# Optimization experiments

Measured on AMD Instinct MI355X. Metric: run time of the kernel, lower is better.

The kernel has to match this reference:

```python
import jax, jax.numpy as jnp
import numpy as np

N_NODES = 50000
N_EDGES = 800000
HIDDEN = 100
NUM_TASKS = 128
NUM_GRAPHS = 2000
ATOM_DIMS = [119, 5, 12, 12, 10, 6, 6, 2, 2]  # OGB full_atom_feature_dims
EPS = 1e-16  # stands in for PyG's clamp(min=0) so that pow(-1) stays finite


def setup_inputs() -> dict:
    key = jax.random.key(0)
    ks = jax.random.split(key, 8)
    x = jax.random.randint(ks[0], (N_NODES, 9), 0, 2, dtype=jnp.int32)
    edge_index = jax.random.randint(ks[1], (2, N_EDGES), 0, N_NODES, dtype=jnp.int32)
    batch = jnp.sort(jax.random.randint(ks[2], (N_NODES,), 0, NUM_GRAPHS, dtype=jnp.int32))
    s = 1.0 / np.sqrt(HIDDEN)
    atom_emb = jax.random.normal(ks[3], (sum(ATOM_DIMS), HIDDEN), jnp.float32)
    W1 = jax.random.normal(ks[4], (HIDDEN, HIDDEN), jnp.float32) * s
    b1 = jnp.zeros((HIDDEN,), jnp.float32)
    W2 = jax.random.normal(ks[5], (HIDDEN, HIDDEN), jnp.float32) * s
    b2 = jnp.zeros((HIDDEN,), jnp.float32)
    Wlin = jax.random.normal(ks[6], (HIDDEN, NUM_TASKS), jnp.float32) * s
    blin = jnp.zeros((NUM_TASKS,), jnp.float32)
    return dict(x=x, edge_index=edge_index, batch=batch, atom_emb=atom_emb,
                W1=W1, b1=b1, W2=W2, b2=b2, Wlin=Wlin, blin=blin)


def reference(x, edge_index, batch, atom_emb, W1, b1, W2, b2, Wlin, blin):
    # --- AtomEncoder: sum of per-feature categorical embeddings ---
    offsets = jnp.asarray(np.concatenate([[0], np.cumsum(ATOM_DIMS)[:-1]]), jnp.int32)
    h = jnp.take(atom_emb, x + offsets[None, :], axis=0).sum(axis=1)  # [N, H]

    # --- GCN normalization with self-loops (gcn_norm, edge_weight=None) ---
    loops = jnp.arange(N_NODES, dtype=edge_index.dtype)
    row = jnp.concatenate([edge_index[0], loops])  # source
    col = jnp.concatenate([edge_index[1], loops])  # target
    ew = jnp.ones(row.shape[0], jnp.float32)
    deg = jax.ops.segment_sum(ew, col, num_segments=N_NODES)  # in-degree incl self-loop
    dinv = jnp.where(deg > 0, deg ** -0.5, 0.0)
    norm = dinv[row] * ew * dinv[col]  # [E+N]
    cnt = jnp.maximum(deg, 1.0)  # messages per target node (for mean)

    def gcn_conv(h, W, b):
        msg = norm[:, None] * (h @ W)[row]  # [E+N, H]
        # PowerMeanAggregation(p=-1): clamp(0,100).pow(-1) -> mean -> clamp(0,100).pow(-1)
        msg = jnp.clip(msg, EPS, 100.0) ** (-1.0)
        agg = jax.ops.segment_sum(msg, col, num_segments=N_NODES) / cnt[:, None]
        return jnp.clip(agg, EPS, 100.0) ** (-1.0) + b

    h = jax.nn.relu(gcn_conv(h, W1, b1))
    h = gcn_conv(h, W2, b2)

    # --- global_mean_pool over batch ---
    gcnt = jax.ops.segment_sum(jnp.ones((N_NODES,), jnp.float32), batch, num_segments=NUM_GRAPHS)
    pooled = jax.ops.segment_sum(h, batch, num_segments=NUM_GRAPHS) / jnp.maximum(gcnt, 1.0)[:, None]

    return pooled @ Wlin + blin  # [NUM_GRAPHS, NUM_TASKS]
```

## Files before the change

### kernel.cpp

```cpp
#include <hip/hip_runtime.h>

#define N_NODES   50000
#define N_EDGES   800000
#define HIDDEN    100
#define NUM_TASKS 128
#define NUM_GRAPHS 2000
#define EPS 1e-16f

static __device__ __forceinline__ float rcp_fast(float v) {
    return __builtin_amdgcn_rcpf(v);
}
static __device__ __forceinline__ float invclip(float v) {
    return rcp_fast(fminf(fmaxf(v, EPS), 100.0f));
}
static __device__ __forceinline__ unsigned pack_bf16x2(float a, float b) {
    unsigned r;
    asm("v_cvt_pk_bf16_f32 %0, %1, %2" : "=v"(r) : "v"(a), "v"(b));
    return r;
}

__global__ void init_kernel(int* __restrict__ deg, int* __restrict__ cursor) {
    int i = blockIdx.x * blockDim.x + threadIdx.x;
    if (i < N_NODES) { deg[i] = 1; cursor[i] = 0; }
}

__global__ void deg_count_kernel(const int* __restrict__ col, int* __restrict__ deg) {
    int e = blockIdx.x * blockDim.x + threadIdx.x;
    if (e < N_EDGES) atomicAdd(&deg[col[e]], 1);
}

__global__ void blk_sum_kernel(const int* __restrict__ deg, int* __restrict__ bsum) {
    int i = blockIdx.x * 256 + threadIdx.x;
    int v = (i < N_NODES) ? (deg[i] - 1) : 0;
#pragma unroll
    for (int off = 32; off > 0; off >>= 1) v += __shfl_down(v, off, 64);
    __shared__ int ws[4];
    if ((threadIdx.x & 63) == 0) ws[threadIdx.x >> 6] = v;
    __syncthreads();
    if (threadIdx.x == 0) bsum[blockIdx.x] = ws[0] + ws[1] + ws[2] + ws[3];
}

__global__ void bsum_scan_kernel(int* __restrict__ bsum, int nblk) {
    __shared__ int buf[256];
    int t = threadIdx.x;
    int v = (t < nblk) ? bsum[t] : 0;
    buf[t] = v;
    __syncthreads();
    for (int off = 1; off < 256; off <<= 1) {
        int x = (t >= off) ? buf[t - off] : 0;
        __syncthreads();
        buf[t] += x;
        __syncthreads();
    }
    if (t < nblk) bsum[t] = buf[t] - v;
}

__global__ void blk_scan_kernel(const int* __restrict__ deg, const int* __restrict__ bbase,
                                int* __restrict__ csr_off, float* __restrict__ dinv) {
    __shared__ int buf[256];
    int t = threadIdx.x;
    int i = blockIdx.x * 256 + t;
    int dv = (i < N_NODES) ? deg[i] : 1;
    int v = (i < N_NODES) ? (dv - 1) : 0;
    buf[t] = v;
    __syncthreads();
    for (int off = 1; off < 256; off <<= 1) {
        int x = (t >= off) ? buf[t - off] : 0;
        __syncthreads();
        buf[t] += x;
        __syncthreads();
    }
    if (i < N_NODES) {
        csr_off[i] = bbase[blockIdx.x] + buf[t] - v;
        dinv[i] = 1.0f / sqrtf((float)dv);
    } else if (i == N_NODES) {
        csr_off[N_NODES] = N_EDGES;
    }
}

__global__ void scatter_kernel(const int* __restrict__ row, const int* __restrict__ col,
                               const int* __restrict__ csr_off, int* __restrict__ cursor,
                               const float* __restrict__ dinv, int2* __restrict__ csr_pack) {
    int e = blockIdx.x * blockDim.x + threadIdx.x;
    if (e >= N_EDGES) return;
    int s = row[e], d = col[e];
    int pos = csr_off[d] + atomicAdd(&cursor[d], 1);
    int2 p;
    p.x = s;
    p.y = __float_as_int(dinv[s] * dinv[d]);
    csr_pack[pos] = p;
}

__global__ void encoder_kernel(const int* __restrict__ x, const float* __restrict__ emb,
                               float* __restrict__ h) {
    int n = blockIdx.x;
    int d = threadIdx.x;
    if (d >= HIDDEN) return;
    const int offs[9] = {0, 119, 124, 136, 148, 158, 164, 170, 172};
    float acc = 0.0f;
#pragma unroll
    for (int f = 0; f < 9; ++f) {
        int idx = x[n * 9 + f] + offs[f];
        acc += emb[idx * HIDDEN + d];
    }
    h[n * HIDDEN + d] = acc;
}

#define MM_NODES 64
#define WL_PAD   10032
__global__ __launch_bounds__(512) void matmul_kernel(const float* __restrict__ h,
                                                     const float* __restrict__ W,
                                                     unsigned* __restrict__ outb) {
    __shared__ float Wl[WL_PAD];
    __shared__ float hl[MM_NODES * HIDDEN];
    int tid = threadIdx.x;
    int nb = blockIdx.x * MM_NODES;

    for (int i = tid; i < WL_PAD; i += 512)
        Wl[i] = (i < HIDDEN * HIDDEN) ? W[i] : 0.0f;
    for (int i = tid; i < MM_NODES * HIDDEN; i += 512) {
        int n = i / HIDDEN;
        hl[i] = (nb + n < N_NODES) ? h[(size_t)(nb + n) * HIDDEN + (i % HIDDEN)] : 0.0f;
    }
    __syncthreads();

    int tx = tid & 31;
    int ty = tid >> 5;

    float4 acc[4];
#pragma unroll
    for (int jn = 0; jn < 4; ++jn) acc[jn] = make_float4(0.f, 0.f, 0.f, 0.f);

    for (int kk = 0; kk < HIDDEN; kk += 4) {
        float hs[4][4];
#pragma unroll
        for (int jn = 0; jn < 4; ++jn) {
            float4 hv = *(const float4*)&hl[(ty + 16 * jn) * HIDDEN + kk];
            hs[jn][0] = hv.x; hs[jn][1] = hv.y; hs[jn][2] = hv.z; hs[jn][3] = hv.w;
        }
#pragma unroll
        for (int dk = 0; dk < 4; ++dk) {
            float4 wv = *(const float4*)&Wl[(kk + dk) * HIDDEN + 4 * tx];
#pragma unroll
            for (int jn = 0; jn < 4; ++jn) {
                acc[jn].x += hs[jn][dk] * wv.x;
                acc[jn].y += hs[jn][dk] * wv.y;
                acc[jn].z += hs[jn][dk] * wv.z;
                acc[jn].w += hs[jn][dk] * wv.w;
            }
        }
    }

    if (tx < 25) {
#pragma unroll
        for (int jn = 0; jn < 4; ++jn) {
            int n = nb + ty + 16 * jn;
            if (n < N_NODES) {
                uint2 pk;
                pk.x = pack_bf16x2(acc[jn].x, acc[jn].y);
                pk.y = pack_bf16x2(acc[jn].z, acc[jn].w);
                *(uint2*)&outb[(size_t)n * 50 + 2 * tx] = pk;
            }
        }
    }
}

__global__ __launch_bounds__(256) void agg_kernel(
        const unsigned* __restrict__ hw16, const int* __restrict__ csr_off,
        const int2* __restrict__ csr_pack, const float* __restrict__ dinv,
        const int* __restrict__ deg, const float* __restrict__ bias,
        float* __restrict__ out, int relu) {
    int wid  = (blockIdx.x * blockDim.x + threadIdx.x) >> 6;
    int lane = threadIdx.x & 63;
    if (wid >= N_NODES) return;
    int n = wid;
    bool act = lane < 50;

    float cnt = (float)deg[n];
    float thr = 100.0f * cnt;
    float dn  = dinv[n];
    float nrm = dn * dn;

    float2 acc;
    if (act) {
        unsigned u = hw16[(size_t)n * 50 + lane];
        acc.x = invclip(nrm * __int_as_float(u << 16));
        acc.y = invclip(nrm * __int_as_float(u & 0xFFFF0000u));
    } else {
        acc.x = 3.0e38f;
        acc.y = 3.0e38f;
    }

    int beg = csr_off[n], end = csr_off[n + 1];
    int i = beg;
    for (; i + 4 <= end; i += 4) {
        int2 p0 = csr_pack[i];
        int2 p1 = csr_pack[i + 1];
        int2 p2 = csr_pack[i + 2];
        int2 p3 = csr_pack[i + 3];
        unsigned u0 = act ? hw16[(size_t)p0.x * 50 + lane] : 0u;
        unsigned u1 = act ? hw16[(size_t)p1.x * 50 + lane] : 0u;
        unsigned u2 = act ? hw16[(size_t)p2.x * 50 + lane] : 0u;
        unsigned u3 = act ? hw16[(size_t)p3.x * 50 + lane] : 0u;
        float w0 = __int_as_float(p0.y), w1 = __int_as_float(p1.y);
        float w2 = __int_as_float(p2.y), w3 = __int_as_float(p3.y);
        acc.x += invclip(w0 * __int_as_float(u0 << 16));
        acc.y += invclip(w0 * __int_as_float(u0 & 0xFFFF0000u));
        acc.x += invclip(w1 * __int_as_float(u1 << 16));
        acc.y += invclip(w1 * __int_as_float(u1 & 0xFFFF0000u));
        acc.x += invclip(w2 * __int_as_float(u2 << 16));
        acc.y += invclip(w2 * __int_as_float(u2 & 0xFFFF0000u));
        acc.x += invclip(w3 * __int_as_float(u3 << 16));
        acc.y += invclip(w3 * __int_as_float(u3 & 0xFFFF0000u));
        if (__all((acc.x >= thr) & (acc.y >= thr))) { i = end; break; }
    }
    for (; i < end; ++i) {
        int2 p = csr_pack[i];
        unsigned u = act ? hw16[(size_t)p.x * 50 + lane] : 0u;
        float w = __int_as_float(p.y);
        acc.x += invclip(w * __int_as_float(u << 16));
        acc.y += invclip(w * __int_as_float(u & 0xFFFF0000u));
    }

    if (act) {
        float rcnt = rcp_fast(cnt);
        float2 o;
        o.x = invclip(acc.x * rcnt) + bias[2 * lane];
        o.y = invclip(acc.y * rcnt) + bias[2 * lane + 1];
        if (relu) { o.x = fmaxf(o.x, 0.f); o.y = fmaxf(o.y, 0.f); }
        *(float2*)&out[(size_t)n * HIDDEN + 2 * lane] = o;
    }
}

__global__ void pool_final_kernel(const float* __restrict__ h, const int* __restrict__ batch,
                                  const float* __restrict__ Wlin, const float* __restrict__ blin,
                                  float* __restrict__ out) {
    int g = blockIdx.x;
    int t = threadIdx.x;
    __shared__ float pl[HIDDEN];

    int lo = 0, hi = N_NODES;
    while (lo < hi) { int mid = (lo + hi) >> 1; if (batch[mid] < g) lo = mid + 1; else hi = mid; }
    int start = lo;
    hi = N_NODES;
    while (lo < hi) { int mid = (lo + hi) >> 1; if (batch[mid] < g + 1) lo = mid + 1; else hi = mid; }
    int end = lo;

    float inv = 1.0f / fmaxf((float)(end - start), 1.0f);
    if (t < HIDDEN) {
        float acc = 0.f;
        for (int n = start; n < end; ++n) acc += h[(size_t)n * HIDDEN + t];
        pl[t] = acc * inv;
    }
    __syncthreads();

    float o = 0.f;
#pragma unroll 4
    for (int j = 0; j < HIDDEN; ++j) o += pl[j] * Wlin[j * NUM_TASKS + t];
    out[(size_t)g * NUM_TASKS + t] = o + blin[t];
}

extern "C" void kernel_launch(void* const* d_in, const int* in_sizes, int n_in,
                              void* d_out, int out_size, void* d_ws, size_t ws_size,
                              hipStream_t stream) {
    const int*   x     = (const int*)d_in[0];
    const int*   ei    = (const int*)d_in[1];
    const int*   batch = (const int*)d_in[2];
    const float* emb   = (const float*)d_in[3];
    const float* W1    = (const float*)d_in[4];
    const float* b1    = (const float*)d_in[5];
    const float* W2    = (const float*)d_in[6];
    const float* b2    = (const float*)d_in[7];
    const float* Wlin  = (const float*)d_in[8];
    const float* blin  = (const float*)d_in[9];
    float* out = (float*)d_out;

    const int* row = ei;
    const int* col = ei + N_EDGES;

    char* ws = (char*)d_ws;
    auto alloc = [&](size_t bytes) -> char* {
        char* p = ws;
        ws += (bytes + 255) & ~(size_t)255;
        return p;
    };
    int*      deg      = (int*)     alloc((size_t)N_NODES * 4);
    int*      cursor   = (int*)     alloc((size_t)N_NODES * 4);
    int*      csr_off  = (int*)     alloc((size_t)(N_NODES + 1) * 4);
    float*    dinv     = (float*)   alloc((size_t)N_NODES * 4);
    int2*     csr_pack = (int2*)    alloc((size_t)N_EDGES * 8);
    float*    bufA     = (float*)   alloc((size_t)N_NODES * HIDDEN * 4);
    unsigned* hw16     = (unsigned*)alloc((size_t)N_NODES * 50 * 4);
    int*      bsum     = (int*)     alloc(256 * 4);

    const int SCAN_BLOCKS = (N_NODES + 255) / 256;

    init_kernel<<<(N_NODES + 255) / 256, 256, 0, stream>>>(deg, cursor);
    deg_count_kernel<<<(N_EDGES + 255) / 256, 256, 0, stream>>>(col, deg);
    blk_sum_kernel<<<SCAN_BLOCKS, 256, 0, stream>>>(deg, bsum);
    bsum_scan_kernel<<<1, 256, 0, stream>>>(bsum, SCAN_BLOCKS);
    blk_scan_kernel<<<SCAN_BLOCKS, 256, 0, stream>>>(deg, bsum, csr_off, dinv);
    scatter_kernel<<<(N_EDGES + 255) / 256, 256, 0, stream>>>(row, col, csr_off, cursor, dinv,
                                                              csr_pack);
    encoder_kernel<<<N_NODES, 128, 0, stream>>>(x, emb, bufA);

    const int MM_BLOCKS = (N_NODES + MM_NODES - 1) / MM_NODES;
    matmul_kernel<<<MM_BLOCKS, 512, 0, stream>>>(bufA, W1, hw16);
    agg_kernel<<<(N_NODES + 3) / 4, 256, 0, stream>>>(hw16, csr_off, csr_pack,
                                                      dinv, deg, b1, bufA, 1);
    matmul_kernel<<<MM_BLOCKS, 512, 0, stream>>>(bufA, W2, hw16);
    agg_kernel<<<(N_NODES + 3) / 4, 256, 0, stream>>>(hw16, csr_off, csr_pack,
                                                      dinv, deg, b2, bufA, 0);

    pool_final_kernel<<<NUM_GRAPHS, 128, 0, stream>>>(bufA, batch, Wlin, blin, out);
}
```

Before: 305.4 us.

## Fuse atom encoder into first matmul, drop early exit, use nontemporal CSR loads

The atom encoder is folded into the first GEMM kernel, so embeddings are built directly in shared memory and the encoder output never round-trips through global memory. The aggregation kernel drops its saturation-based early-exit vote and reads CSR pairs with nontemporal 64-bit loads. It also writes output with nontemporal stores and launches 128-thread blocks of two wavefronts. Removing the early exit means every edge is always processed, which may cost time on nodes whose sums saturate early.

```diff
diff --git a/kernel.cpp b/kernel.cpp
--- a/kernel.cpp
+++ b/kernel.cpp
@@ -91,39 +91,11 @@
     csr_pack[pos] = p;
 }
 
-__global__ void encoder_kernel(const int* __restrict__ x, const float* __restrict__ emb,
-                               float* __restrict__ h) {
-    int n = blockIdx.x;
-    int d = threadIdx.x;
-    if (d >= HIDDEN) return;
-    const int offs[9] = {0, 119, 124, 136, 148, 158, 164, 170, 172};
-    float acc = 0.0f;
-#pragma unroll
-    for (int f = 0; f < 9; ++f) {
-        int idx = x[n * 9 + f] + offs[f];
-        acc += emb[idx * HIDDEN + d];
-    }
-    h[n * HIDDEN + d] = acc;
-}
-
 #define MM_NODES 64
 #define WL_PAD   10032
-__global__ __launch_bounds__(512) void matmul_kernel(const float* __restrict__ h,
-                                                     const float* __restrict__ W,
-                                                     unsigned* __restrict__ outb) {
-    __shared__ float Wl[WL_PAD];
-    __shared__ float hl[MM_NODES * HIDDEN];
-    int tid = threadIdx.x;
-    int nb = blockIdx.x * MM_NODES;
-
-    for (int i = tid; i < WL_PAD; i += 512)
-        Wl[i] = (i < HIDDEN * HIDDEN) ? W[i] : 0.0f;
-    for (int i = tid; i < MM_NODES * HIDDEN; i += 512) {
-        int n = i / HIDDEN;
-        hl[i] = (nb + n < N_NODES) ? h[(size_t)(nb + n) * HIDDEN + (i % HIDDEN)] : 0.0f;
-    }
-    __syncthreads();
-
+
+static __device__ __forceinline__ void gemm_tile(const float* Wl, const float* hl,
+                                                 unsigned* __restrict__ outb, int nb, int tid) {
     int tx = tid & 31;
     int ty = tid >> 5;
 
@@ -165,7 +137,60 @@
     }
 }
 
-__global__ __launch_bounds__(256) void agg_kernel(
+__global__ __launch_bounds__(512) void mm_enc_kernel(const int* __restrict__ x,
+                                                     const float* __restrict__ emb,
+                                                     const float* __restrict__ W,
+                                                     unsigned* __restrict__ outb) {
+    __shared__ float Wl[WL_PAD];
+    __shared__ float hl[MM_NODES * HIDDEN];
+    __shared__ int   xl[MM_NODES * 9];
+    int tid = threadIdx.x;
+    int nb = blockIdx.x * MM_NODES;
+
+    for (int i = tid; i < WL_PAD; i += 512)
+        Wl[i] = (i < HIDDEN * HIDDEN) ? W[i] : 0.0f;
+    for (int i = tid; i < MM_NODES * 9; i += 512) {
+        int n = i / 9, gn = nb + n;
+        xl[i] = (gn < N_NODES) ? x[gn * 9 + (i - n * 9)] : -1;
+    }
+    __syncthreads();
+
+    const int offs[9] = {0, 119, 124, 136, 148, 158, 164, 170, 172};
+    for (int i = tid; i < MM_NODES * HIDDEN; i += 512) {
+        int n = i / HIDDEN, d = i - n * HIDDEN;
+        float acc = 0.0f;
+        if (xl[n * 9] >= 0) {
+#pragma unroll
+            for (int f = 0; f < 9; ++f)
+                acc += emb[(size_t)(xl[n * 9 + f] + offs[f]) * HIDDEN + d];
+        }
+        hl[i] = acc;
+    }
+    __syncthreads();
+
+    gemm_tile(Wl, hl, outb, nb, tid);
+}
+
+__global__ __launch_bounds__(512) void matmul_kernel(const float* __restrict__ h,
+                                                     const float* __restrict__ W,
+                                                     unsigned* __restrict__ outb) {
+    __shared__ float Wl[WL_PAD];
+    __shared__ float hl[MM_NODES * HIDDEN];
+    int tid = threadIdx.x;
+    int nb = blockIdx.x * MM_NODES;
+
+    for (int i = tid; i < WL_PAD; i += 512)
+        Wl[i] = (i < HIDDEN * HIDDEN) ? W[i] : 0.0f;
+    for (int i = tid; i < MM_NODES * HIDDEN; i += 512) {
+        int n = i / HIDDEN;
+        hl[i] = (nb + n < N_NODES) ? h[(size_t)(nb + n) * HIDDEN + (i % HIDDEN)] : 0.0f;
+    }
+    __syncthreads();
+
+    gemm_tile(Wl, hl, outb, nb, tid);
+}
+
+__global__ __launch_bounds__(128) void agg_kernel(
         const unsigned* __restrict__ hw16, const int* __restrict__ csr_off,
         const int2* __restrict__ csr_pack, const float* __restrict__ dinv,
         const int* __restrict__ deg, const float* __restrict__ bias,
@@ -177,33 +202,33 @@
     bool act = lane < 50;
 
     float cnt = (float)deg[n];
-    float thr = 100.0f * cnt;
     float dn  = dinv[n];
     float nrm = dn * dn;
 
-    float2 acc;
+    float2 acc = make_float2(0.f, 0.f);
     if (act) {
         unsigned u = hw16[(size_t)n * 50 + lane];
         acc.x = invclip(nrm * __int_as_float(u << 16));
         acc.y = invclip(nrm * __int_as_float(u & 0xFFFF0000u));
-    } else {
-        acc.x = 3.0e38f;
-        acc.y = 3.0e38f;
-    }
-
+    }
+
+    const long long* packs = (const long long*)csr_pack;
     int beg = csr_off[n], end = csr_off[n + 1];
     int i = beg;
     for (; i + 4 <= end; i += 4) {
-        int2 p0 = csr_pack[i];
-        int2 p1 = csr_pack[i + 1];
-        int2 p2 = csr_pack[i + 2];
-        int2 p3 = csr_pack[i + 3];
-        unsigned u0 = act ? hw16[(size_t)p0.x * 50 + lane] : 0u;
-        unsigned u1 = act ? hw16[(size_t)p1.x * 50 + lane] : 0u;
-        unsigned u2 = act ? hw16[(size_t)p2.x * 50 + lane] : 0u;
-        unsigned u3 = act ? hw16[(size_t)p3.x * 50 + lane] : 0u;
-        float w0 = __int_as_float(p0.y), w1 = __int_as_float(p1.y);
-        float w2 = __int_as_float(p2.y), w3 = __int_as_float(p3.y);
+        long long q0 = __builtin_nontemporal_load(&packs[i]);
+        long long q1 = __builtin_nontemporal_load(&packs[i + 1]);
+        long long q2 = __builtin_nontemporal_load(&packs[i + 2]);
+        long long q3 = __builtin_nontemporal_load(&packs[i + 3]);
+        int s0 = (int)q0, s1 = (int)q1, s2 = (int)q2, s3 = (int)q3;
+        unsigned u0 = act ? hw16[(size_t)s0 * 50 + lane] : 0u;
+        unsigned u1 = act ? hw16[(size_t)s1 * 50 + lane] : 0u;
+        unsigned u2 = act ? hw16[(size_t)s2 * 50 + lane] : 0u;
+        unsigned u3 = act ? hw16[(size_t)s3 * 50 + lane] : 0u;
+        float w0 = __int_as_float((int)(q0 >> 32));
+        float w1 = __int_as_float((int)(q1 >> 32));
+        float w2 = __int_as_float((int)(q2 >> 32));
+        float w3 = __int_as_float((int)(q3 >> 32));
         acc.x += invclip(w0 * __int_as_float(u0 << 16));
         acc.y += invclip(w0 * __int_as_float(u0 & 0xFFFF0000u));
         acc.x += invclip(w1 * __int_as_float(u1 << 16));
@@ -212,23 +237,24 @@
         acc.y += invclip(w2 * __int_as_float(u2 & 0xFFFF0000u));
         acc.x += invclip(w3 * __int_as_float(u3 << 16));
         acc.y += invclip(w3 * __int_as_float(u3 & 0xFFFF0000u));
-        if (__all((acc.x >= thr) & (acc.y >= thr))) { i = end; break; }
     }
     for (; i < end; ++i) {
-        int2 p = csr_pack[i];
-        unsigned u = act ? hw16[(size_t)p.x * 50 + lane] : 0u;
-        float w = __int_as_float(p.y);
+        long long q = __builtin_nontemporal_load(&packs[i]);
+        int s = (int)q;
+        unsigned u = act ? hw16[(size_t)s * 50 + lane] : 0u;
+        float w = __int_as_float((int)(q >> 32));
         acc.x += invclip(w * __int_as_float(u << 16));
         acc.y += invclip(w * __int_as_float(u & 0xFFFF0000u));
     }
 
     if (act) {
         float rcnt = rcp_fast(cnt);
-        float2 o;
-        o.x = invclip(acc.x * rcnt) + bias[2 * lane];
-        o.y = invclip(acc.y * rcnt) + bias[2 * lane + 1];
-        if (relu) { o.x = fmaxf(o.x, 0.f); o.y = fmaxf(o.y, 0.f); }
-        *(float2*)&out[(size_t)n * HIDDEN + 2 * lane] = o;
+        float ox = invclip(acc.x * rcnt) + bias[2 * lane];
+        float oy = invclip(acc.y * rcnt) + bias[2 * lane + 1];
+        if (relu) { ox = fmaxf(ox, 0.f); oy = fmaxf(oy, 0.f); }
+        unsigned long long w = (unsigned long long)__float_as_uint(ox)
+                             | ((unsigned long long)__float_as_uint(oy) << 32);
+        __builtin_nontemporal_store(w, (unsigned long long*)&out[(size_t)n * HIDDEN + 2 * lane]);
     }
 }
 
@@ -302,14 +328,13 @@
     blk_scan_kernel<<<SCAN_BLOCKS, 256, 0, stream>>>(deg, bsum, csr_off, dinv);
     scatter_kernel<<<(N_EDGES + 255) / 256, 256, 0, stream>>>(row, col, csr_off, cursor, dinv,
                                                               csr_pack);
-    encoder_kernel<<<N_NODES, 128, 0, stream>>>(x, emb, bufA);
 
     const int MM_BLOCKS = (N_NODES + MM_NODES - 1) / MM_NODES;
-    matmul_kernel<<<MM_BLOCKS, 512, 0, stream>>>(bufA, W1, hw16);
-    agg_kernel<<<(N_NODES + 3) / 4, 256, 0, stream>>>(hw16, csr_off, csr_pack,
+    mm_enc_kernel<<<MM_BLOCKS, 512, 0, stream>>>(x, emb, W1, hw16);
+    agg_kernel<<<(N_NODES + 1) / 2, 128, 0, stream>>>(hw16, csr_off, csr_pack,
                                                       dinv, deg, b1, bufA, 1);
     matmul_kernel<<<MM_BLOCKS, 512, 0, stream>>>(bufA, W2, hw16);
-    agg_kernel<<<(N_NODES + 3) / 4, 256, 0, stream>>>(hw16, csr_off, csr_pack,
+    agg_kernel<<<(N_NODES + 1) / 2, 128, 0, stream>>>(hw16, csr_off, csr_pack,
                                                       dinv, deg, b2, bufA, 0);
 
     pool_final_kernel<<<NUM_GRAPHS, 128, 0, stream>>>(bufA, batch, Wlin, blin, out);
```

Result: slower. 322.1 us (+5.5%).
